# Performance work log

Hardware: AMD Instinct MI355X
Metric: run time of the kernel (lower is better)

Reference implementation:

```python
import jax, jax.numpy as jnp
import numpy as np

B, H, N, F, P, NODE = 64, 168, 512, 8, 24, 0


def _lstm(x, k, rk, b, return_sequences):
    # x: (B, T, Fin); keras LSTM gate order i, f, g(c), o
    Bx = x.shape[0]
    U = rk.shape[0]
    h0 = jnp.zeros((Bx, U), x.dtype)

    def step(carry, xt):
        h, c = carry
        z = xt @ k + h @ rk + b
        i, f, g, o = jnp.split(z, 4, axis=-1)
        c = jax.nn.sigmoid(f) * c + jax.nn.sigmoid(i) * jnp.tanh(g)
        h = jax.nn.sigmoid(o) * jnp.tanh(c)
        return (h, c), h

    (_, _), hs = jax.lax.scan(step, (h0, h0), jnp.swapaxes(x, 0, 1))
    return jnp.swapaxes(hs, 0, 1) if return_sequences else hs[-1]


def _node_summaries(inputs):
    # inputs: (B, H, N, F). Per-(b,n) temporal stats over H of feature 0.
    x0 = inputs[..., 0]                      # (B, H, N)
    mean_full = x0.mean(axis=1)              # (B, N)
    mean_half = x0[:, H // 2:].mean(axis=1)
    std_full = x0.std(axis=1)                # population std (ddof=0), like tf
    std_half = x0[:, H // 2:].std(axis=1)
    c = x0 - mean_full[:, None, :]
    m2 = (c * c).mean(axis=1)
    m3 = (c ** 3).mean(axis=1)
    m4 = (c ** 4).mean(axis=1)
    skew = jnp.nan_to_num(m3 / m2 ** 1.5)    # scipy.stats.skew (biased)
    kurt = jnp.nan_to_num(m4 / (m2 * m2) - 3.0)  # scipy Fisher kurtosis
    t = jnp.arange(H, dtype=x0.dtype)
    tc = t - t.mean()
    slope = jnp.nan_to_num(jnp.einsum('h,bhn->bn', tc, x0) / (tc * tc).sum())
    return jnp.stack([mean_full, mean_half, std_full, std_half, skew, kurt, slope], axis=2)  # (B, N, 7)


def reference(inputs, adj, w_gcn1, b_gcn1, w_gcn2, b_gcn2, w_conv1, b_conv1,
              w_conv2, b_conv2, k_lstm1, rk_lstm1, b_lstm1, k_lstm2, rk_lstm2,
              b_lstm2, w_out, b_out):
    nf = _node_summaries(inputs)                                   # (B, N, 7)
    # GraphConv: relu(A @ X @ W + b)
    h = jax.nn.relu(jnp.einsum('nm,bmc->bnc', adj, nf @ w_gcn1) + b_gcn1)
    g = jax.nn.relu(jnp.einsum('nm,bmc->bnc', adj, h @ w_gcn2) + b_gcn2)   # (B, N, 16)
    # Conv1D channels_first: channels = N, steps = 16
    dn = ('NCH', 'HIO', 'NCH')
    c1 = jax.lax.conv_general_dilated(g, w_conv1, (1,), 'SAME', dimension_numbers=dn) + b_conv1[None, :, None]  # (B,4,16)
    p = c1.reshape(B, 4, 8, 2).mean(axis=-1)                        # AveragePooling1D(2)  (B,4,8)
    c2 = jax.lax.conv_general_dilated(p, w_conv2, (1,), 'SAME', dimension_numbers=dn) + b_conv2[None, :, None]  # (B,4,8)
    gcn_out = jnp.concatenate([c2.reshape(B, -1), p.reshape(B, -1)], axis=-1)  # skip connection, (B, 64)
    # LSTM stack on the selected node's time series
    seq = inputs[:, :, NODE, :]                                     # (B, H, F)
    l1 = _lstm(seq, k_lstm1, rk_lstm1, b_lstm1, True)
    l2 = _lstm(l1, k_lstm2, rk_lstm2, b_lstm2, False)               # (B, 128)
    out = jnp.concatenate([gcn_out, l2], axis=-1)                   # (B, 192); dropout is identity at inference
    return out @ w_out + b_out                                      # (B, P)


def setup_inputs() -> dict:
    key = jax.random.key(0)
    ks = jax.random.split(key, 16)
    s = 0.05
    return {
        'inputs': jax.random.normal(ks[0], (B, H, N, F), jnp.float32),
        'adj': jax.random.uniform(ks[1], (N, N), jnp.float32) / N,
        'w_gcn1': jax.random.normal(ks[2], (7, 32), jnp.float32) * s,
        'b_gcn1': jnp.zeros((32,), jnp.float32),
        'w_gcn2': jax.random.normal(ks[3], (32, 16), jnp.float32) * s,
        'b_gcn2': jnp.zeros((16,), jnp.float32),
        'w_conv1': jax.random.normal(ks[4], (3, N, 4), jnp.float32) * s,
        'b_conv1': jnp.zeros((4,), jnp.float32),
        'w_conv2': jax.random.normal(ks[5], (3, 4, 4), jnp.float32) * s,
        'b_conv2': jnp.zeros((4,), jnp.float32),
        'k_lstm1': jax.random.normal(ks[6], (F, 512), jnp.float32) * s,
        'rk_lstm1': jax.random.normal(ks[7], (128, 512), jnp.float32) * s,
        'b_lstm1': jnp.zeros((512,), jnp.float32),
        'k_lstm2': jax.random.normal(ks[8], (128, 512), jnp.float32) * s,
        'rk_lstm2': jax.random.normal(ks[9], (128, 512), jnp.float32) * s,
        'b_lstm2': jnp.zeros((512,), jnp.float32),
        'w_out': jax.random.normal(ks[10], (192, P), jnp.float32) * s,
        'b_out': jnp.zeros((P,), jnp.float32),
    }
```

## Files before the change

kernel.cpp:

```cpp
#include <hip/hip_runtime.h>
#include <cstdint>
#include <cstddef>

#define BB 64
#define HH 168
#define NN 512
#define FF 8
#define UL 128
#define GD 512

__device__ __forceinline__ float sigf(float x){ return 1.0f/(1.0f+__expf(-x)); }
__device__ __forceinline__ float tanhfast(float x){ return 1.0f - 2.0f/(1.0f+__expf(2.0f*x)); }
__device__ __forceinline__ float frcp(float x){ return __builtin_amdgcn_rcpf(x); }

__global__ __launch_bounds__(256) void k_sum(const float* __restrict__ in, float* __restrict__ ps){
  int bid = blockIdx.x;
  int b = bid>>2, nh = (bid>>1)&1, hh = bid&1;
  int n = nh*256 + threadIdx.x;
  int h0 = hh*84;
  const float* p = in + ((size_t)(b*HH + h0)*NN + n)*FF;
  float s1=0.f,s2=0.f,s3=0.f,s4=0.f,st=0.f;
  #pragma unroll 4
  for(int h=0;h<84;++h){
    float x = p[(size_t)h*NN*FF];
    float hc = (float)(h+h0) - 83.5f;
    s1 += x;
    float x2 = x*x;
    s2 += x2;
    s3 += x2*x;
    s4 += x2*x2;
    st += hc*x;
  }
  float* o = ps + ((size_t)((b*NN+n)*2 + hh))*8;
  o[0]=s1; o[1]=s2; o[2]=s3; o[3]=s4; o[4]=st;
}

__global__ __launch_bounds__(256) void k_sumc(const float* __restrict__ ps, float* __restrict__ nf){
  int idx = blockIdx.x*256 + threadIdx.x;
  const float* a = ps + (size_t)idx*16;
  const float* c2 = a + 8;
  float s1 = a[0]+c2[0], s2 = a[1]+c2[1], s3 = a[2]+c2[2], s4 = a[3]+c2[3], st = a[4]+c2[4];
  float s1h = c2[0], s2h = c2[1];
  const float iH = 1.0f/168.0f, iHh = 1.0f/84.0f;
  float mean = s1*iH, meanh = s1h*iHh;
  float ex2 = s2*iH, ex3 = s3*iH, ex4 = s4*iH;
  float m2 = ex2 - mean*mean;
  float m3 = ex3 - 3.0f*mean*ex2 + 2.0f*mean*mean*mean;
  float m4 = ex4 - 4.0f*mean*ex3 + 6.0f*mean*mean*ex2 - 3.0f*mean*mean*mean*mean;
  m2 = fmaxf(m2, 0.0f);
  float stdf = sqrtf(m2);
  float m2h = fmaxf(s2h*iHh - meanh*meanh, 0.0f);
  float stdh = sqrtf(m2h);
  float denom = m2*stdf;
  float skew = denom > 0.0f ? m3/denom : 0.0f;
  float kurt = m2 > 0.0f ? (m4/(m2*m2) - 3.0f) : 0.0f;
  float slope = st * (1.0f/395122.0f);
  float* o = nf + (size_t)idx*7;
  o[0]=mean; o[1]=meanh; o[2]=stdf; o[3]=stdh; o[4]=skew; o[5]=kurt; o[6]=slope;
}

__global__ __launch_bounds__(256) void k_gcn1(const float* __restrict__ nf, const float* __restrict__ adj,
        const float* __restrict__ w1, const float* __restrict__ b1, float* __restrict__ h1){
  __shared__ float t_s[NN*32];
  __shared__ float adj_s[128*68];
  int b = blockIdx.x>>2, n0 = (blockIdx.x&3)*128;
  int tid = threadIdx.x;
  {
    int c = tid&31;
    float w1c[7];
    #pragma unroll
    for(int k=0;k<7;++k) w1c[k] = w1[k*32+c];
    for(int idx=tid; idx<NN*32; idx+=256){
      int m = idx>>5;
      const float* nfp = nf + (size_t)(b*NN+m)*7;
      float acc = 0.f;
      #pragma unroll
      for(int k=0;k<7;++k) acc += nfp[k]*w1c[k];
      t_s[idx] = acc;
    }
  }
  int c2 = tid&15, nl = tid>>4;
  float acc[8][2];
  #pragma unroll
  for(int j=0;j<8;++j){acc[j][0]=0.f;acc[j][1]=0.f;}
  for(int mt=0; mt<8; ++mt){
    __syncthreads();
    for(int idx=tid; idx<128*64; idx+=256){
      int r = idx>>6, cc = idx&63;
      adj_s[r*68+cc] = adj[(size_t)(n0+r)*NN + mt*64 + cc];
    }
    __syncthreads();
    for(int mm=0; mm<64; mm+=4){
      float2 tv[4];
      #pragma unroll
      for(int q=0;q<4;++q) tv[q] = *(const float2*)&t_s[(mt*64+mm+q)*32 + 2*c2];
      #pragma unroll
      for(int j=0;j<8;++j){
        float4 a4 = *(const float4*)&adj_s[(nl+16*j)*68 + mm];
        acc[j][0] += a4.x*tv[0].x + a4.y*tv[1].x + a4.z*tv[2].x + a4.w*tv[3].x;
        acc[j][1] += a4.x*tv[0].y + a4.y*tv[1].y + a4.z*tv[2].y + a4.w*tv[3].y;
      }
    }
  }
  float bb0 = b1[2*c2], bb1 = b1[2*c2+1];
  #pragma unroll
  for(int j=0;j<8;++j){
    int n = n0 + nl + 16*j;
    float2 v;
    v.x = fmaxf(acc[j][0]+bb0, 0.0f);
    v.y = fmaxf(acc[j][1]+bb1, 0.0f);
    *(float2*)&h1[(size_t)(b*NN+n)*32 + 2*c2] = v;
  }
}

__global__ __launch_bounds__(256) void k_gcn2(const float* __restrict__ h1, const float* __restrict__ adj,
        const float* __restrict__ w2, const float* __restrict__ b2, float* __restrict__ g){
  __shared__ float t_s[NN*16];
  __shared__ float adj_s[128*68];
  int b = blockIdx.x>>2, n0 = (blockIdx.x&3)*128;
  int tid = threadIdx.x;
  {
    int jh = tid&7;
    float w2c0[32], w2c1[32];
    #pragma unroll
    for(int c=0;c<32;++c){ w2c0[c] = w2[c*16+2*jh]; w2c1[c] = w2[c*16+2*jh+1]; }
    for(int idx=tid; idx<NN*8; idx+=256){
      int m = idx>>3;
      const float4* hp = (const float4*)(h1 + (size_t)(b*NN+m)*32);
      float a0=0.f, a1=0.f;
      #pragma unroll
      for(int q=0;q<8;++q){
        float4 hv = hp[q];
        a0 += hv.x*w2c0[4*q] + hv.y*w2c0[4*q+1] + hv.z*w2c0[4*q+2] + hv.w*w2c0[4*q+3];
        a1 += hv.x*w2c1[4*q] + hv.y*w2c1[4*q+1] + hv.z*w2c1[4*q+2] + hv.w*w2c1[4*q+3];
      }
      t_s[m*16+2*jh] = a0;
      t_s[m*16+2*jh+1] = a1;
    }
  }
  int j = tid&15, nl = tid>>4;
  float acc[8];
  #pragma unroll
  for(int q=0;q<8;++q) acc[q]=0.f;
  for(int mt=0; mt<8; ++mt){
    __syncthreads();
    for(int idx=tid; idx<128*64; idx+=256){
      int r = idx>>6, cc = idx&63;
      adj_s[r*68+cc] = adj[(size_t)(n0+r)*NN + mt*64 + cc];
    }
    __syncthreads();
    for(int mm=0; mm<64; mm+=4){
      float tv[4];
      #pragma unroll
      for(int q=0;q<4;++q) tv[q] = t_s[(mt*64+mm+q)*16 + j];
      #pragma unroll
      for(int q=0;q<8;++q){
        float4 a4 = *(const float4*)&adj_s[(nl+16*q)*68 + mm];
        acc[q] += a4.x*tv[0] + a4.y*tv[1] + a4.z*tv[2] + a4.w*tv[3];
      }
    }
  }
  float bbj = b2[j];
  #pragma unroll
  for(int q=0;q<8;++q){
    int n = n0 + nl + 16*q;
    g[(size_t)(b*NN+n)*16 + j] = fmaxf(acc[q]+bbj, 0.0f);
  }
}

__global__ __launch_bounds__(256) void k_conv(const float* __restrict__ g, const float* __restrict__ wc1,
        const float* __restrict__ bc1, const float* __restrict__ wc2, const float* __restrict__ bc2,
        float* __restrict__ feat){
  __shared__ float g_s[NN*16];
  __shared__ float w1_s[3*NN*4];
  __shared__ float c1p[4][4][16];
  __shared__ float c1_s[4][16];
  __shared__ float p_s[4][8];
  int b = blockIdx.x, tid = threadIdx.x;
  for(int idx=tid; idx<NN*16; idx+=256) g_s[idx] = g[(size_t)b*NN*16 + idx];
  for(int idx=tid; idx<3*NN*4; idx+=256) w1_s[idx] = wc1[idx];
  __syncthreads();
  {
    int q = tid>>6, p = tid&63, o = p>>4, x = p&15;
    int c0 = q*128;
    float acc = 0.f;
    #pragma unroll
    for(int k=0;k<3;++k){
      int xx = x + k - 1;
      if(xx>=0 && xx<16){
        #pragma unroll 4
        for(int c=c0;c<c0+128;++c) acc += g_s[c*16+xx]*w1_s[(k*NN+c)*4+o];
      }
    }
    c1p[q][o][x] = acc;
  }
  __syncthreads();
  if(tid<64){
    int o = tid>>4, x = tid&15;
    c1_s[o][x] = c1p[0][o][x]+c1p[1][o][x]+c1p[2][o][x]+c1p[3][o][x] + bc1[o];
  }
  __syncthreads();
  if(tid<32){
    int oo = tid>>3, xp = tid&7;
    float pv = 0.5f*(c1_s[oo][2*xp]+c1_s[oo][2*xp+1]);
    p_s[oo][xp] = pv;
    feat[b*192 + 32 + oo*8 + xp] = pv;
  }
  __syncthreads();
  if(tid<32){
    int oo = tid>>3, x2 = tid&7;
    float a2 = bc2[oo];
    #pragma unroll
    for(int k=0;k<3;++k){
      int xx = x2 + k - 1;
      if(xx>=0 && xx<8){
        #pragma unroll
        for(int c=0;c<4;++c) a2 += p_s[c][xx]*wc2[(k*4+c)*4+oo];
      }
    }
    feat[b*192 + oo*8 + x2] = a2;
  }
}

__global__ __launch_bounds__(512,2) void k_lstm1(const float* __restrict__ in, const float* __restrict__ k1,
        const float* __restrict__ rk1, const float* __restrict__ b1, float* __restrict__ l1){
  __shared__ float seq_s[HH*FF];
  __shared__ float hbuf[2][UL];
  int b = blockIdx.x, tid = threadIdx.x;
  int w = tid>>6, l = tid&63, gate = l>>4, us = l&15;
  int u = w*16 + us;
  int col = gate*128 + u;
  float wr[UL];
  #pragma unroll
  for(int m=0;m<UL;++m) wr[m] = rk1[m*GD + col];
  float wkx[FF];
  #pragma unroll
  for(int f=0;f<FF;++f) wkx[f] = k1[f*GD + col];
  float bz = b1[col];
  bool isg = (gate==2);
  float Ac = isg?1.f:0.f, Bc = isg?-2.f:1.f, Sc = isg?2.f:-1.f;
  for(int idx=tid; idx<HH*FF; idx+=512)
    seq_s[idx] = in[(size_t)(b*HH + (idx>>3))*NN*FF + (idx&7)];
  if(tid<UL){ hbuf[0][tid] = 0.0f; }
  float c = 0.0f;
  __syncthreads();
  float* hr = &hbuf[0][0];
  float* hw = &hbuf[1][0];
  #pragma unroll 1
  for(int t=0;t<HH;++t){
    float4 x0 = *(const float4*)&seq_s[t*FF];
    float4 x1 = *(const float4*)&seq_s[t*FF+4];
    float z0 = bz + x0.x*wkx[0]+x0.y*wkx[1];
    float z1 = x0.z*wkx[2]+x0.w*wkx[3];
    float z2 = x1.x*wkx[4]+x1.y*wkx[5];
    float z3 = x1.z*wkx[6]+x1.w*wkx[7];
    const float4* h4 = (const float4*)hr;
    #pragma unroll
    for(int j=0;j<32;++j){
      float4 hv = h4[j];
      z0 += hv.x*wr[4*j];
      z1 += hv.y*wr[4*j+1];
      z2 += hv.z*wr[4*j+2];
      z3 += hv.w*wr[4*j+3];
    }
    float z = (z0+z1)+(z2+z3);
    float act = Ac + Bc*frcp(1.0f + __expf(Sc*z));
    float r16 = __shfl_xor(act, 16);
    float r32 = __shfl_xor(act, 32);
    float r48 = __shfl_xor(r16, 32);
    float ia = gate==0?act : gate==1?r16 : gate==2?r32 : r48;
    float fa = gate==0?r16 : gate==1?act : gate==2?r48 : r32;
    float ga = gate==0?r32 : gate==1?r48 : gate==2?act : r16;
    float oa = gate==0?r48 : gate==1?r32 : gate==2?r16 : act;
    c = fa*c + ia*ga;
    float th = 1.0f - 2.0f*frcp(1.0f + __expf(2.0f*c));
    float hn = oa*th;
    if(gate==0){
      hw[u] = hn;
      l1[((size_t)b*HH + t)*UL + u] = hn;
    }
    __syncthreads();
    float* tmp = hr; hr = hw; hw = tmp;
  }
}

__global__ __launch_bounds__(256) void k_zin2(const float* __restrict__ l1, const float* __restrict__ k2,
        const float* __restrict__ b2, float* __restrict__ zin){
  __shared__ float l_s[21*UL];
  int b = blockIdx.x>>3, t0 = (blockIdx.x&7)*21;
  int tid = threadIdx.x;
  for(int idx=tid; idx<21*UL; idx+=256)
    l_s[idx] = l1[((size_t)b*HH + t0 + (idx>>7))*UL + (idx&127)];
  __syncthreads();
  float acc0[21], acc1[21];
  #pragma unroll
  for(int q=0;q<21;++q){acc0[q]=0.f;acc1[q]=0.f;}
  for(int j=0;j<UL;j+=4){
    float kv00=k2[j*GD+tid],     kv01=k2[(j+1)*GD+tid],     kv02=k2[(j+2)*GD+tid],     kv03=k2[(j+3)*GD+tid];
    float kv10=k2[j*GD+tid+256], kv11=k2[(j+1)*GD+tid+256], kv12=k2[(j+2)*GD+tid+256], kv13=k2[(j+3)*GD+tid+256];
    #pragma unroll
    for(int q=0;q<21;++q){
      float4 lv = *(const float4*)&l_s[q*UL + j];
      acc0[q] += lv.x*kv00 + lv.y*kv01 + lv.z*kv02 + lv.w*kv03;
      acc1[q] += lv.x*kv10 + lv.y*kv11 + lv.z*kv12 + lv.w*kv13;
    }
  }
  float bb0 = b2[tid], bb1 = b2[tid+256];
  #pragma unroll
  for(int q=0;q<21;++q){
    zin[((size_t)b*HH + t0 + q)*GD + tid]       = acc0[q] + bb0;
    zin[((size_t)b*HH + t0 + q)*GD + tid + 256] = acc1[q] + bb1;
  }
}

__global__ __launch_bounds__(512,2) void k_lstm2(const float* __restrict__ zin, const float* __restrict__ rk2,
        float* __restrict__ feat){
  __shared__ float hbuf[2][UL];
  int b = blockIdx.x, tid = threadIdx.x;
  int w = tid>>6, l = tid&63, gate = l>>4, us = l&15;
  int u = w*16 + us;
  int col = gate*128 + u;
  float wr[UL];
  #pragma unroll
  for(int m=0;m<UL;++m) wr[m] = rk2[m*GD + col];
  bool isg = (gate==2);
  float Ac = isg?1.f:0.f, Bc = isg?-2.f:1.f, Sc = isg?2.f:-1.f;
  if(tid<UL){ hbuf[0][tid] = 0.0f; }
  float c = 0.0f;
  float zc = zin[((size_t)b*HH)*GD + col];
  __syncthreads();
  float* hr = &hbuf[0][0];
  float* hw = &hbuf[1][0];
  #pragma unroll 1
  for(int t=0;t<HH;++t){
    float nz = 0.f;
    if(t+1<HH) nz = zin[((size_t)b*HH+t+1)*GD + col];
    float z0 = zc, z1 = 0.f, z2 = 0.f, z3 = 0.f;
    const float4* h4 = (const float4*)hr;
    #pragma unroll
    for(int j=0;j<32;++j){
      float4 hv = h4[j];
      z0 += hv.x*wr[4*j];
      z1 += hv.y*wr[4*j+1];
      z2 += hv.z*wr[4*j+2];
      z3 += hv.w*wr[4*j+3];
    }
    float z = (z0+z1)+(z2+z3);
    float act = Ac + Bc*frcp(1.0f + __expf(Sc*z));
    float r16 = __shfl_xor(act, 16);
    float r32 = __shfl_xor(act, 32);
    float r48 = __shfl_xor(r16, 32);
    float ia = gate==0?act : gate==1?r16 : gate==2?r32 : r48;
    float fa = gate==0?r16 : gate==1?act : gate==2?r48 : r32;
    float ga = gate==0?r32 : gate==1?r48 : gate==2?act : r16;
    float oa = gate==0?r48 : gate==1?r32 : gate==2?r16 : act;
    c = fa*c + ia*ga;
    float th = 1.0f - 2.0f*frcp(1.0f + __expf(2.0f*c));
    float hn = oa*th;
    if(gate==0){
      hw[u] = hn;
      if(t==HH-1) feat[b*192 + 64 + u] = hn;
    }
    __syncthreads();
    float* tmp = hr; hr = hw; hw = tmp;
    zc = nz;
  }
}

__global__ __launch_bounds__(256) void k_out(const float* __restrict__ feat, const float* __restrict__ wo,
        const float* __restrict__ bo, float* __restrict__ out){
  int idx = blockIdx.x*256 + threadIdx.x;
  if(idx >= BB*24) return;
  int b = idx/24, p = idx - b*24;
  float a0 = bo[p], a1 = 0.f, a2 = 0.f, a3 = 0.f;
  const float* f = feat + b*192;
  for(int k=0;k<192;k+=4){
    a0 += f[k]*wo[k*24+p];
    a1 += f[k+1]*wo[(k+1)*24+p];
    a2 += f[k+2]*wo[(k+2)*24+p];
    a3 += f[k+3]*wo[(k+3)*24+p];
  }
  out[idx] = (a0+a1)+(a2+a3);
}

extern "C" void kernel_launch(void* const* d_in, const int* in_sizes, int n_in,
                              void* d_out, int out_size, void* d_ws, size_t ws_size,
                              hipStream_t stream){
  const float* inp = (const float*)d_in[0];
  const float* adj = (const float*)d_in[1];
  const float* w1  = (const float*)d_in[2];
  const float* b1  = (const float*)d_in[3];
  const float* w2  = (const float*)d_in[4];
  const float* b2  = (const float*)d_in[5];
  const float* wc1 = (const float*)d_in[6];
  const float* bc1 = (const float*)d_in[7];
  const float* wc2 = (const float*)d_in[8];
  const float* bc2 = (const float*)d_in[9];
  const float* k1  = (const float*)d_in[10];
  const float* rk1 = (const float*)d_in[11];
  const float* bl1 = (const float*)d_in[12];
  const float* k2  = (const float*)d_in[13];
  const float* rk2 = (const float*)d_in[14];
  const float* bl2 = (const float*)d_in[15];
  const float* wo  = (const float*)d_in[16];
  const float* bo  = (const float*)d_in[17];
  float* out = (float*)d_out;
  float* ws = (float*)d_ws;

  float* ps   = ws;
  float* nf   = ps + 524288;
  float* h1   = nf + 229376;
  float* g    = h1 + 1048576;
  float* feat = g  + 524288;
  float* l1   = feat + 12288;
  float* zin  = l1 + 1376256;

  k_sum  <<<dim3(256), dim3(256), 0, stream>>>(inp, ps);
  k_sumc <<<dim3(128), dim3(256), 0, stream>>>(ps, nf);
  k_gcn1 <<<dim3(256), dim3(256), 0, stream>>>(nf, adj, w1, b1, h1);
  k_gcn2 <<<dim3(256), dim3(256), 0, stream>>>(h1, adj, w2, b2, g);
  k_conv <<<dim3(64),  dim3(256), 0, stream>>>(g, wc1, bc1, wc2, bc2, feat);
  k_lstm1<<<dim3(64),  dim3(512), 0, stream>>>(inp, k1, rk1, bl1, l1);
  k_zin2 <<<dim3(512), dim3(256), 0, stream>>>(l1, k2, bl2, zin);
  k_lstm2<<<dim3(64),  dim3(512), 0, stream>>>(zin, rk2, feat);
  k_out  <<<dim3(6),   dim3(256), 0, stream>>>(feat, wo, bo, out);
}
```

Measured before the change: 520.2 us.

## Split LSTM recurrence K-dimension across lanes and hoist layer-1 input projection

The recurrent matvec now uses 1024 threads per batch. Each lane computes a 16-element slice of the hidden-state dot product for four gate columns, and the partial sums are combined with xor shuffles. This shortens the per-step serial chain of FMAs and LDS reads and lowers register pressure from 128 weights per thread. The layer-1 input projection is moved into a separate parallel precompute kernel so that both layers share one recurrence kernel. The cost is extra shuffles per step, an extra kernel launch with zin memory traffic, and larger block-wide barriers.

```diff
diff --git a/kernel.cpp b/kernel.cpp
--- a/kernel.cpp
+++ b/kernel.cpp
@@ -9,8 +9,6 @@
 #define UL 128
 #define GD 512
 
-__device__ __forceinline__ float sigf(float x){ return 1.0f/(1.0f+__expf(-x)); }
-__device__ __forceinline__ float tanhfast(float x){ return 1.0f - 2.0f/(1.0f+__expf(2.0f*x)); }
 __device__ __forceinline__ float frcp(float x){ return __builtin_amdgcn_rcpf(x); }
 
 __global__ __launch_bounds__(256) void k_sum(const float* __restrict__ in, float* __restrict__ ps){
@@ -222,48 +220,119 @@
   }
 }
 
-__global__ __launch_bounds__(512,2) void k_lstm1(const float* __restrict__ in, const float* __restrict__ k1,
-        const float* __restrict__ rk1, const float* __restrict__ b1, float* __restrict__ l1){
-  __shared__ float seq_s[HH*FF];
-  __shared__ float hbuf[2][UL];
+__global__ __launch_bounds__(256) void k_xk1(const float* __restrict__ in, const float* __restrict__ k1,
+        const float* __restrict__ b1, float* __restrict__ zin){
+  __shared__ float x_s[21*FF];
+  int b = blockIdx.x>>3, t0 = (blockIdx.x&7)*21;
+  int tid = threadIdx.x;
+  for(int idx=tid; idx<21*FF; idx+=256)
+    x_s[idx] = in[(size_t)(b*HH + t0 + (idx>>3))*NN*FF + (idx&7)];
+  __syncthreads();
+  float acc0[21], acc1[21];
+  #pragma unroll
+  for(int q=0;q<21;++q){acc0[q]=0.f;acc1[q]=0.f;}
+  #pragma unroll
+  for(int j=0;j<FF;++j){
+    float kv0 = k1[j*GD + tid];
+    float kv1 = k1[j*GD + tid + 256];
+    #pragma unroll
+    for(int q=0;q<21;++q){
+      float xv = x_s[q*FF + j];
+      acc0[q] += xv*kv0;
+      acc1[q] += xv*kv1;
+    }
+  }
+  float bb0 = b1[tid], bb1 = b1[tid+256];
+  #pragma unroll
+  for(int q=0;q<21;++q){
+    zin[((size_t)b*HH + t0 + q)*GD + tid]       = acc0[q] + bb0;
+    zin[((size_t)b*HH + t0 + q)*GD + tid + 256] = acc1[q] + bb1;
+  }
+}
+
+__global__ __launch_bounds__(256) void k_zin2(const float* __restrict__ l1, const float* __restrict__ k2,
+        const float* __restrict__ b2, float* __restrict__ zin){
+  __shared__ float l_s[21*UL];
+  int b = blockIdx.x>>3, t0 = (blockIdx.x&7)*21;
+  int tid = threadIdx.x;
+  for(int idx=tid; idx<21*UL; idx+=256)
+    l_s[idx] = l1[((size_t)b*HH + t0 + (idx>>7))*UL + (idx&127)];
+  __syncthreads();
+  float acc0[21], acc1[21];
+  #pragma unroll
+  for(int q=0;q<21;++q){acc0[q]=0.f;acc1[q]=0.f;}
+  for(int j=0;j<UL;j+=4){
+    float kv00=k2[j*GD+tid],     kv01=k2[(j+1)*GD+tid],     kv02=k2[(j+2)*GD+tid],     kv03=k2[(j+3)*GD+tid];
+    float kv10=k2[j*GD+tid+256], kv11=k2[(j+1)*GD+tid+256], kv12=k2[(j+2)*GD+tid+256], kv13=k2[(j+3)*GD+tid+256];
+    #pragma unroll
+    for(int q=0;q<21;++q){
+      float4 lv = *(const float4*)&l_s[q*UL + j];
+      acc0[q] += lv.x*kv00 + lv.y*kv01 + lv.z*kv02 + lv.w*kv03;
+      acc1[q] += lv.x*kv10 + lv.y*kv11 + lv.z*kv12 + lv.w*kv13;
+    }
+  }
+  float bb0 = b2[tid], bb1 = b2[tid+256];
+  #pragma unroll
+  for(int q=0;q<21;++q){
+    zin[((size_t)b*HH + t0 + q)*GD + tid]       = acc0[q] + bb0;
+    zin[((size_t)b*HH + t0 + q)*GD + tid + 256] = acc1[q] + bb1;
+  }
+}
+
+__global__ __launch_bounds__(1024) __attribute__((amdgpu_waves_per_eu(4,4)))
+void k_rec(const float* __restrict__ zin, const float* __restrict__ rk,
+           float* __restrict__ oseq, float* __restrict__ olast, int writeSeq){
+  __shared__ float hbuf[2][8*20];
   int b = blockIdx.x, tid = threadIdx.x;
-  int w = tid>>6, l = tid&63, gate = l>>4, us = l&15;
-  int u = w*16 + us;
-  int col = gate*128 + u;
-  float wr[UL];
-  #pragma unroll
-  for(int m=0;m<UL;++m) wr[m] = rk1[m*GD + col];
-  float wkx[FF];
-  #pragma unroll
-  for(int f=0;f<FF;++f) wkx[f] = k1[f*GD + col];
-  float bz = b1[col];
+  int w = tid>>6, l = tid&63;
+  int gate = l>>4;
+  int ks = l&7;
+  int b3 = (l>>3)&1;
+  int cbase = gate*128 + w*8 + b3*4;
+  int col = cbase + (l&3);
+  int u = w*8 + b3*4 + (l&3);
+  bool q0 = (l&1)!=0, q1 = (l&2)!=0;
+  bool wr = (gate==0) && ((l&4)==0);
+
+  float4 w4[16];
+  #pragma unroll
+  for(int k=0;k<16;++k)
+    w4[k] = *(const float4*)(rk + (size_t)(ks*16+k)*GD + cbase);
+
   bool isg = (gate==2);
   float Ac = isg?1.f:0.f, Bc = isg?-2.f:1.f, Sc = isg?2.f:-1.f;
-  for(int idx=tid; idx<HH*FF; idx+=512)
-    seq_s[idx] = in[(size_t)(b*HH + (idx>>3))*NN*FF + (idx&7)];
-  if(tid<UL){ hbuf[0][tid] = 0.0f; }
+
+  if(tid<UL) hbuf[0][(tid>>4)*20 + (tid&15)] = 0.0f;
   float c = 0.0f;
-  __syncthreads();
-  float* hr = &hbuf[0][0];
-  float* hw = &hbuf[1][0];
+  float zc = zin[(size_t)b*HH*GD + col];
+  __syncthreads();
+
+  int cur = 0;
   #pragma unroll 1
   for(int t=0;t<HH;++t){
-    float4 x0 = *(const float4*)&seq_s[t*FF];
-    float4 x1 = *(const float4*)&seq_s[t*FF+4];
-    float z0 = bz + x0.x*wkx[0]+x0.y*wkx[1];
-    float z1 = x0.z*wkx[2]+x0.w*wkx[3];
-    float z2 = x1.x*wkx[4]+x1.y*wkx[5];
-    float z3 = x1.z*wkx[6]+x1.w*wkx[7];
-    const float4* h4 = (const float4*)hr;
-    #pragma unroll
-    for(int j=0;j<32;++j){
-      float4 hv = h4[j];
-      z0 += hv.x*wr[4*j];
-      z1 += hv.y*wr[4*j+1];
-      z2 += hv.z*wr[4*j+2];
-      z3 += hv.w*wr[4*j+3];
-    }
-    float z = (z0+z1)+(z2+z3);
+    float nz = 0.f;
+    if(t+1<HH) nz = zin[((size_t)b*HH + t+1)*GD + col];
+    const float4* hq = (const float4*)&hbuf[cur][ks*20];
+    float p0=0.f,p1=0.f,p2=0.f,p3=0.f;
+    #pragma unroll
+    for(int j=0;j<4;++j){
+      float4 hv = hq[j];
+      p0 += hv.x*w4[4*j].x + hv.y*w4[4*j+1].x + hv.z*w4[4*j+2].x + hv.w*w4[4*j+3].x;
+      p1 += hv.x*w4[4*j].y + hv.y*w4[4*j+1].y + hv.z*w4[4*j+2].y + hv.w*w4[4*j+3].y;
+      p2 += hv.x*w4[4*j].z + hv.y*w4[4*j+1].z + hv.z*w4[4*j+2].z + hv.w*w4[4*j+3].z;
+      p3 += hv.x*w4[4*j].w + hv.y*w4[4*j+1].w + hv.z*w4[4*j+2].w + hv.w*w4[4*j+3].w;
+    }
+    p0 += __shfl_xor(p0,4); p1 += __shfl_xor(p1,4);
+    p2 += __shfl_xor(p2,4); p3 += __shfl_xor(p3,4);
+    float send0 = q0 ? p0 : p1;
+    float send1 = q0 ? p2 : p3;
+    float r0 = __shfl_xor(send0, 1);
+    float r1 = __shfl_xor(send1, 1);
+    float s0 = (q0 ? p1 : p0) + r0;
+    float s1v = (q0 ? p3 : p2) + r1;
+    float send2 = q1 ? s0 : s1v;
+    float r2 = __shfl_xor(send2, 2);
+    float z = zc + (q1 ? s1v : s0) + r2;
     float act = Ac + Bc*frcp(1.0f + __expf(Sc*z));
     float r16 = __shfl_xor(act, 16);
     float r32 = __shfl_xor(act, 32);
@@ -275,94 +344,13 @@
     c = fa*c + ia*ga;
     float th = 1.0f - 2.0f*frcp(1.0f + __expf(2.0f*c));
     float hn = oa*th;
-    if(gate==0){
-      hw[u] = hn;
-      l1[((size_t)b*HH + t)*UL + u] = hn;
+    if(wr){
+      hbuf[cur^1][(u>>4)*20 + (u&15)] = hn;
+      if(writeSeq) oseq[((size_t)b*HH + t)*UL + u] = hn;
+      else if(t==HH-1) olast[b*192 + 64 + u] = hn;
     }
     __syncthreads();
-    float* tmp = hr; hr = hw; hw = tmp;
-  }
-}
-
-__global__ __launch_bounds__(256) void k_zin2(const float* __restrict__ l1, const float* __restrict__ k2,
-        const float* __restrict__ b2, float* __restrict__ zin){
-  __shared__ float l_s[21*UL];
-  int b = blockIdx.x>>3, t0 = (blockIdx.x&7)*21;
-  int tid = threadIdx.x;
-  for(int idx=tid; idx<21*UL; idx+=256)
-    l_s[idx] = l1[((size_t)b*HH + t0 + (idx>>7))*UL + (idx&127)];
-  __syncthreads();
-  float acc0[21], acc1[21];
-  #pragma unroll
-  for(int q=0;q<21;++q){acc0[q]=0.f;acc1[q]=0.f;}
-  for(int j=0;j<UL;j+=4){
-    float kv00=k2[j*GD+tid],     kv01=k2[(j+1)*GD+tid],     kv02=k2[(j+2)*GD+tid],     kv03=k2[(j+3)*GD+tid];
-    float kv10=k2[j*GD+tid+256], kv11=k2[(j+1)*GD+tid+256], kv12=k2[(j+2)*GD+tid+256], kv13=k2[(j+3)*GD+tid+256];
-    #pragma unroll
-    for(int q=0;q<21;++q){
-      float4 lv = *(const float4*)&l_s[q*UL + j];
-      acc0[q] += lv.x*kv00 + lv.y*kv01 + lv.z*kv02 + lv.w*kv03;
-      acc1[q] += lv.x*kv10 + lv.y*kv11 + lv.z*kv12 + lv.w*kv13;
-    }
-  }
-  float bb0 = b2[tid], bb1 = b2[tid+256];
-  #pragma unroll
-  for(int q=0;q<21;++q){
-    zin[((size_t)b*HH + t0 + q)*GD + tid]       = acc0[q] + bb0;
-    zin[((size_t)b*HH + t0 + q)*GD + tid + 256] = acc1[q] + bb1;
-  }
-}
-
-__global__ __launch_bounds__(512,2) void k_lstm2(const float* __restrict__ zin, const float* __restrict__ rk2,
-        float* __restrict__ feat){
-  __shared__ float hbuf[2][UL];
-  int b = blockIdx.x, tid = threadIdx.x;
-  int w = tid>>6, l = tid&63, gate = l>>4, us = l&15;
-  int u = w*16 + us;
-  int col = gate*128 + u;
-  float wr[UL];
-  #pragma unroll
-  for(int m=0;m<UL;++m) wr[m] = rk2[m*GD + col];
-  bool isg = (gate==2);
-  float Ac = isg?1.f:0.f, Bc = isg?-2.f:1.f, Sc = isg?2.f:-1.f;
-  if(tid<UL){ hbuf[0][tid] = 0.0f; }
-  float c = 0.0f;
-  float zc = zin[((size_t)b*HH)*GD + col];
-  __syncthreads();
-  float* hr = &hbuf[0][0];
-  float* hw = &hbuf[1][0];
-  #pragma unroll 1
-  for(int t=0;t<HH;++t){
-    float nz = 0.f;
-    if(t+1<HH) nz = zin[((size_t)b*HH+t+1)*GD + col];
-    float z0 = zc, z1 = 0.f, z2 = 0.f, z3 = 0.f;
-    const float4* h4 = (const float4*)hr;
-    #pragma unroll
-    for(int j=0;j<32;++j){
-      float4 hv = h4[j];
-      z0 += hv.x*wr[4*j];
-      z1 += hv.y*wr[4*j+1];
-      z2 += hv.z*wr[4*j+2];
-      z3 += hv.w*wr[4*j+3];
-    }
-    float z = (z0+z1)+(z2+z3);
-    float act = Ac + Bc*frcp(1.0f + __expf(Sc*z));
-    float r16 = __shfl_xor(act, 16);
-    float r32 = __shfl_xor(act, 32);
-    float r48 = __shfl_xor(r16, 32);
-    float ia = gate==0?act : gate==1?r16 : gate==2?r32 : r48;
-    float fa = gate==0?r16 : gate==1?act : gate==2?r48 : r32;
-    float ga = gate==0?r32 : gate==1?r48 : gate==2?act : r16;
-    float oa = gate==0?r48 : gate==1?r32 : gate==2?r16 : act;
-    c = fa*c + ia*ga;
-    float th = 1.0f - 2.0f*frcp(1.0f + __expf(2.0f*c));
-    float hn = oa*th;
-    if(gate==0){
-      hw[u] = hn;
-      if(t==HH-1) feat[b*192 + 64 + u] = hn;
-    }
-    __syncthreads();
-    float* tmp = hr; hr = hw; hw = tmp;
+    cur ^= 1;
     zc = nz;
   }
 }
@@ -420,8 +408,9 @@
   k_gcn1 <<<dim3(256), dim3(256), 0, stream>>>(nf, adj, w1, b1, h1);
   k_gcn2 <<<dim3(256), dim3(256), 0, stream>>>(h1, adj, w2, b2, g);
   k_conv <<<dim3(64),  dim3(256), 0, stream>>>(g, wc1, bc1, wc2, bc2, feat);
-  k_lstm1<<<dim3(64),  dim3(512), 0, stream>>>(inp, k1, rk1, bl1, l1);
+  k_xk1  <<<dim3(512), dim3(256), 0, stream>>>(inp, k1, bl1, zin);
+  k_rec  <<<dim3(64),  dim3(1024),0, stream>>>(zin, rk1, l1, feat, 1);
   k_zin2 <<<dim3(512), dim3(256), 0, stream>>>(l1, k2, bl2, zin);
-  k_lstm2<<<dim3(64),  dim3(512), 0, stream>>>(zin, rk2, feat);
+  k_rec  <<<dim3(64),  dim3(1024),0, stream>>>(zin, rk2, l1, feat, 0);
   k_out  <<<dim3(6),   dim3(256), 0, stream>>>(feat, wo, bo, out);
 }
```

Result: faster. 476.9 us (-8.3%).
